# Optimization experiments

Hardware: AMD Instinct MI355X
Metric: run time of the kernel (lower is better)

Reference implementation:

```python
import jax, jax.numpy as jnp
import numpy as np
import math

B, L, I, H = 32, 2048, 64, 512
HALF = H // 2
DT = 0.05
RHO = 0.99
INPUT_SCALING = 1.0
STD = 1.0
GAMMA_MIN, GAMMA_MAX = 0.5, 1.0
EPS_MIN, EPS_MAX = 0.5, 1.0


def setup_inputs() -> dict:
    key = jax.random.key(0)
    ks = jax.random.split(key, 7)
    x = jax.random.normal(ks[0], (B, L, I), dtype=jnp.float32)
    x2h = jax.random.uniform(ks[1], (I, H), dtype=jnp.float32) * INPUT_SCALING
    h2h = 2.0 * (2.0 * jax.random.uniform(ks[2], (H, H), dtype=jnp.float32) - 1.0)
    # spectral_norm_scaling: rescale so largest singular value == rho
    h2h = h2h * (RHO / jnp.linalg.norm(h2h, ord=2))
    bias = (2.0 * jax.random.uniform(ks[3], (H,), dtype=jnp.float32) - 1.0) * INPUT_SCALING
    gamma = jax.random.uniform(ks[4], (H,), dtype=jnp.float32) * (GAMMA_MAX - GAMMA_MIN) + GAMMA_MIN
    epsilon = jax.random.uniform(ks[5], (H,), dtype=jnp.float32) * (EPS_MAX - EPS_MIN) + EPS_MIN
    # RandomFourierFeature: W_sin = W_cos, shape [half_dim, in_dim]
    W_rff = jax.random.normal(ks[6], (HALF, H), dtype=jnp.float32) * STD
    return {"x": x, "x2h": x2h, "h2h": h2h, "bias": bias,
            "gamma": gamma, "epsilon": epsilon, "W_rff": W_rff}


def _run(x, x2h, h2h, bias, gamma, epsilon, W_rff):
    b = x.shape[0]
    inv_sqrt_half = 1.0 / math.sqrt(HALF)

    def step(carry, xt):
        hy, hz, zsum = carry
        pre = jnp.tanh(xt @ x2h + hy @ h2h + bias)          # [B,H]
        hz = hz + DT * (pre - gamma * hy - epsilon * hz)
        hy = hy + DT * hz
        wx = hy @ W_rff.T                                   # [B,HALF]
        z = jnp.concatenate([jnp.cos(wx), jnp.sin(wx)], axis=-1) * inv_sqrt_half
        return (hy, hz, zsum + z), None

    hy0 = jnp.zeros((b, H), dtype=x.dtype)
    hz0 = jnp.zeros((b, H), dtype=x.dtype)
    zsum0 = jnp.zeros((b, H), dtype=x.dtype)
    (hy, hz, zsum), _ = jax.lax.scan(step, (hy0, hz0, zsum0), jnp.swapaxes(x, 0, 1))
    mu = zsum / x.shape[1]  # mean over time of per-step RFF states
    return mu, hy


def reference(x, x2h, h2h, bias, gamma, epsilon, W_rff):
    return _run(x, x2h, h2h, bias, gamma, epsilon, W_rff)
```

## Files before the change

### kernel.cpp

```cpp
#include <hip/hip_runtime.h>
#include <math.h>

#define Bz 32
#define Lz 2048
#define Iz 64
#define Hz 512
#define HALFz 256
#define DTz 0.05f
#define NMEM 8
#define TPB 512

typedef unsigned long long u64;

__device__ __forceinline__ bool tagok(u64 v, unsigned tag) {
  u64 want = (u64)tag | ((u64)tag << 48);
  return ((v ^ want) & 0xFFFF00000000FFFFull) == 0ull;
}
__device__ __forceinline__ u64 packv(float f, unsigned tag) {
  return (u64)tag | ((u64)__float_as_uint(f) << 16) | ((u64)tag << 48);
}
__device__ __forceinline__ float unpackv(u64 v) {
  return __uint_as_float((unsigned)(v >> 16));
}

__device__ __forceinline__ u64 load_sc0(const u64* p) {
  u64 r;
  asm volatile("global_load_dwordx2 %0, %1, off sc0\n\t"
               "s_waitcnt vmcnt(0)"
               : "=&v"(r) : "v"(p) : "memory");
  return r;
}
__device__ __forceinline__ void store_sc0(u64* p, u64 v) {
  asm volatile("global_store_dwordx2 %0, %1, off sc0"
               :: "v"(p), "v"(v) : "memory");
}

__global__ __launch_bounds__(TPB, 2) void coesn_sc0(
    const float* __restrict__ x, const float* __restrict__ x2h,
    const float* __restrict__ h2h, const float* __restrict__ bias,
    const float* __restrict__ gam, const float* __restrict__ eps,
    const float* __restrict__ W_rff, u64* __restrict__ Xb,
    u64* __restrict__ Yb, float* __restrict__ out) {
  __shared__ __align__(16) float hyf[2][Hz];
  __shared__ __align__(16) float xb[2][Iz];

  const int b  = blockIdx.x & 31;
  const int m  = blockIdx.x >> 5;
  const int u  = threadIdx.x;
  const int w  = u >> 6;
  const int l  = u & 63;
  const int c0 = m * 64;
  const int j  = ((l & 1) << 2) | (l & 2) | ((l >> 2) & 1);
  const int mycol = c0 + w * 8 + j;
  const int rloc = u >> 4, kseg = u & 15;

  float wreg[8][8];
  {
    const float* hrow = h2h + (size_t)(8 * l) * Hz + c0 + 8 * w;
    #pragma unroll
    for (int r = 0; r < 8; ++r) {
      float4 v0 = *(const float4*)(hrow + (size_t)r * Hz);
      float4 v1 = *(const float4*)(hrow + (size_t)r * Hz + 4);
      wreg[r][0] = v0.x; wreg[r][1] = v0.y; wreg[r][2] = v0.z; wreg[r][3] = v0.w;
      wreg[r][4] = v1.x; wreg[r][5] = v1.y; wreg[r][6] = v1.z; wreg[r][7] = v1.w;
    }
  }
  float xreg[8];
  {
    float4 v0 = *(const float4*)(x2h + (size_t)l * Hz + c0 + 8 * w);
    float4 v1 = *(const float4*)(x2h + (size_t)l * Hz + c0 + 8 * w + 4);
    xreg[0] = v0.x; xreg[1] = v0.y; xreg[2] = v0.z; xreg[3] = v0.w;
    xreg[4] = v1.x; xreg[5] = v1.y; xreg[6] = v1.z; xreg[7] = v1.w;
  }
  float wr[32];
  {
    const float* wp = W_rff + (size_t)(m * 32 + rloc) * Hz + kseg * 32;
    #pragma unroll
    for (int i = 0; i < 32; ++i) wr[i] = wp[i];
  }

  const float bu = bias[mycol];
  const float gu = gam[mycol];
  const float eu = eps[mycol];
  float hy = 0.f, hz = 0.f, zc = 0.f, zs = 0.f;
  hyf[0][u] = 0.f;
  if (u < 16) ((float4*)xb[0])[u] = ((const float4*)(x + (size_t)b * Lz * Iz))[u];
  __syncthreads();

  auto rff_acc = [&](const float* hsrc) {
    float acc = 0.f;
    const float4* hp = (const float4*)hsrc;
    #pragma unroll
    for (int i = 0; i < 8; ++i) {
      int q = kseg * 8 + i;
      float4 h4 = hp[q ^ ((q >> 3) & 7)];
      acc = fmaf(h4.x, wr[4 * i], acc);
      acc = fmaf(h4.y, wr[4 * i + 1], acc);
      acc = fmaf(h4.z, wr[4 * i + 2], acc);
      acc = fmaf(h4.w, wr[4 * i + 3], acc);
    }
    acc += __shfl_xor(acc, 1); acc += __shfl_xor(acc, 2);
    acc += __shfl_xor(acc, 4); acc += __shfl_xor(acc, 8);
    float sv, cv;
    __sincosf(acc, &sv, &cv);
    zc += cv; zs += sv;
  };

  for (int t = 0; t < Lz; ++t) {
    const int cur = t & 1, nxt = cur ^ 1;

    if (u < 16 && t + 1 < Lz)
      ((float4*)xb[nxt])[u] =
          ((const float4*)(x + ((size_t)b * Lz + (t + 1)) * Iz))[u];

    float hv[8];
    {
      const float4* hp = (const float4*)hyf[cur];
      int q0 = 2 * l, q1 = 2 * l + 1;
      float4 h0 = hp[q0 ^ ((q0 >> 3) & 7)];
      float4 h1 = hp[q1 ^ ((q1 >> 3) & 7)];
      hv[0] = h0.x; hv[1] = h0.y; hv[2] = h0.z; hv[3] = h0.w;
      hv[4] = h1.x; hv[5] = h1.y; hv[6] = h1.z; hv[7] = h1.w;
    }
    float a[8] = {0.f, 0.f, 0.f, 0.f, 0.f, 0.f, 0.f, 0.f};
    #pragma unroll
    for (int r = 0; r < 8; ++r) {
      float h = hv[r];
      #pragma unroll
      for (int c = 0; c < 8; ++c) a[c] = fmaf(h, wreg[r][c], a[c]);
    }
    {
      float xv = xb[cur][l];
      #pragma unroll
      for (int c = 0; c < 8; ++c) a[c] = fmaf(xv, xreg[c], a[c]);
    }
    #pragma unroll
    for (int i = 0; i < 4; ++i) {
      float snd = (l & 1) ? a[i] : a[i + 4];
      float rcv = __shfl_xor(snd, 1);
      a[i] = ((l & 1) ? a[i + 4] : a[i]) + rcv;
    }
    #pragma unroll
    for (int i = 0; i < 2; ++i) {
      float snd = (l & 2) ? a[i] : a[i + 2];
      float rcv = __shfl_xor(snd, 2);
      a[i] = ((l & 2) ? a[i + 2] : a[i]) + rcv;
    }
    float s;
    {
      float snd = (l & 4) ? a[0] : a[1];
      float rcv = __shfl_xor(snd, 4);
      s = ((l & 4) ? a[1] : a[0]) + rcv;
    }
    s += __shfl_xor(s, 8); s += __shfl_xor(s, 16); s += __shfl_xor(s, 32);

    s += bu;
    float e2 = __expf(s + s);
    float pre = 1.f - 2.f * __builtin_amdgcn_rcpf(e2 + 1.f);
    float hzn = fmaf(DTz, pre - gu * hy - eu * hz, hz);
    hy = fmaf(DTz, hzn, hy);
    hz = hzn;

    const unsigned tag = (unsigned)(t + 1);
    u64* XA = Xb + ((size_t)nxt * Bz + b) * Hz;
    u64* YA = Yb + ((size_t)nxt * Bz + b) * Hz;

    if (l < 8) {
      u64 pv = packv(hy, tag);
      store_sc0(XA + mycol, pv);
      __hip_atomic_store(YA + mycol, pv, __ATOMIC_RELAXED,
                         __HIP_MEMORY_SCOPE_AGENT);
      int q = mycol >> 2;
      hyf[nxt][((q ^ ((q >> 3) & 7)) << 2) | (mycol & 3)] = hy;
    }

    u64 spec = 0;
    if (w != m) {
      asm volatile("global_load_dwordx2 %0, %1, off sc0"
                   : "=&v"(spec) : "v"(XA + u) : "memory");
    }

    if (t > 0) rff_acc(hyf[cur]);

    if (w != m) {
      asm volatile("s_waitcnt vmcnt(0)" : "+v"(spec) :: "memory");
      u64 v = spec;
      if (!tagok(v, tag)) {
        int it = 0;
        for (;;) {
          v = load_sc0(XA + u);
          if (tagok(v, tag)) break;
          if (it >= 2) {
            v = __hip_atomic_load(YA + u, __ATOMIC_RELAXED,
                                  __HIP_MEMORY_SCOPE_AGENT);
            if (tagok(v, tag)) break;
          }
          if (++it > (1 << 20)) break;
        }
      }
      int q = u >> 2;
      hyf[nxt][((q ^ ((q >> 3) & 7)) << 2) | (u & 3)] = unpackv(v);
    }
    __syncthreads();
  }

  rff_acc(hyf[0]);

  if (l < 8) out[(size_t)Bz * Hz + (size_t)b * Hz + mycol] = hy;
  if (kseg == 0) {
    const float sc = 0.0625f / 2048.f;
    out[(size_t)b * Hz + m * 32 + rloc] = zc * sc;
    out[(size_t)b * Hz + HALFz + m * 32 + rloc] = zs * sc;
  }
}

#define FMA4(P, S, W) do { (P).x = fmaf((S), (W).x, (P).x); (P).y = fmaf((S), (W).y, (P).y); \
                           (P).z = fmaf((S), (W).z, (P).z); (P).w = fmaf((S), (W).w, (P).w); } while(0)

__global__ __launch_bounds__(512) void coesn_scan_fb(
    const float* __restrict__ x, const float* __restrict__ x2h,
    const float* __restrict__ h2h, const float* __restrict__ bias,
    const float* __restrict__ gam, const float* __restrict__ eps,
    const float* __restrict__ W_rff, float* __restrict__ out) {
  const int b = blockIdx.x;
  const int u = threadIdx.x;
  __shared__ __align__(16) float hy_lds[Hz];
  __shared__ __align__(16) float x_lds[Iz];
  __shared__ float4 part[4][128];
  __shared__ float wx_lds[HALFz];

  float hy = 0.f, hz = 0.f, zsum = 0.f;
  const float bu = bias[u];
  const float gu = gam[u];
  const float eu = eps[u];

  const int kq = u >> 7;
  const int g  = u & 127;
  const int jj = u >> 2;
  const int ks = u & 3;

  const float4* __restrict__ H4 = (const float4*)h2h;
  const float4* __restrict__ X2 = (const float4*)x2h;
  const float4* __restrict__ W4 = (const float4*)W_rff;
  const float4* __restrict__ XG = (const float4*)x;
  const float4* hy4 = (const float4*)hy_lds;

  hy_lds[u] = 0.f;
  if (u < 16) ((float4*)x_lds)[u] = XG[(long)b * Lz * 16 + u];
  __syncthreads();

  for (int t = 0; t < Lz; ++t) {
    float4 p = make_float4(0.f, 0.f, 0.f, 0.f);
    {
      const float4* hp = (const float4*)&hy_lds[kq << 7];
      #pragma unroll 8
      for (int k4 = 0; k4 < 32; ++k4) {
        float4 hv = hp[k4];
        const float4* wr2 = &H4[(size_t)((kq << 7) + (k4 << 2)) * 128 + g];
        float4 w0 = wr2[0]; float4 w1 = wr2[128]; float4 w2 = wr2[256]; float4 w3 = wr2[384];
        FMA4(p, hv.x, w0); FMA4(p, hv.y, w1); FMA4(p, hv.z, w2); FMA4(p, hv.w, w3);
      }
      const float4* xp = (const float4*)&x_lds[kq << 4];
      #pragma unroll
      for (int k4 = 0; k4 < 4; ++k4) {
        float4 xv = xp[k4];
        const float4* wr2 = &X2[(size_t)((kq << 4) + (k4 << 2)) * 128 + g];
        float4 w0 = wr2[0]; float4 w1 = wr2[128]; float4 w2 = wr2[256]; float4 w3 = wr2[384];
        FMA4(p, xv.x, w0); FMA4(p, xv.y, w1); FMA4(p, xv.z, w2); FMA4(p, xv.w, w3);
      }
    }
    part[kq][g] = p;
    __syncthreads();
    {
      const float* pp = (const float*)part;
      float s = (pp[u] + pp[512 + u]) + (pp[1024 + u] + pp[1536 + u]);
      float pre = tanhf(s + bu);
      float hzn = fmaf(DTz, pre - gu * hy - eu * hz, hz);
      hy = fmaf(DTz, hzn, hy);
      hz = hzn;
      hy_lds[u] = hy;
      if (u < 16 && t + 1 < Lz)
        ((float4*)x_lds)[u] = XG[((long)b * Lz + (t + 1)) * 16 + u];
    }
    __syncthreads();
    {
      float4 acc0 = make_float4(0.f,0.f,0.f,0.f), acc1 = make_float4(0.f,0.f,0.f,0.f);
      #pragma unroll 4
      for (int it = 0; it < 32; ++it) {
        int k4 = (it << 2) + ks;
        float4 hv = hy4[k4];
        float4 w0 = W4[(size_t)jj * 128 + k4];
        float4 w1 = W4[(size_t)(jj + 128) * 128 + k4];
        acc0.x = fmaf(hv.x, w0.x, acc0.x); acc0.y = fmaf(hv.y, w0.y, acc0.y);
        acc0.z = fmaf(hv.z, w0.z, acc0.z); acc0.w = fmaf(hv.w, w0.w, acc0.w);
        acc1.x = fmaf(hv.x, w1.x, acc1.x); acc1.y = fmaf(hv.y, w1.y, acc1.y);
        acc1.z = fmaf(hv.z, w1.z, acc1.z); acc1.w = fmaf(hv.w, w1.w, acc1.w);
      }
      float a0 = (acc0.x + acc0.y) + (acc0.z + acc0.w);
      float a1 = (acc1.x + acc1.y) + (acc1.z + acc1.w);
      a0 += __shfl_xor(a0, 1); a0 += __shfl_xor(a0, 2);
      a1 += __shfl_xor(a1, 1); a1 += __shfl_xor(a1, 2);
      if (ks == 0) { wx_lds[jj] = a0; wx_lds[jj + 128] = a1; }
    }
    __syncthreads();
    {
      float v = wx_lds[u & 255];
      zsum += (u < HALFz) ? cosf(v) : sinf(v);
    }
  }
  out[(long)b * Hz + u] = zsum * (0.0625f / 2048.f);
  out[(long)Bz * Hz + (long)b * Hz + u] = hy;
}

extern "C" void kernel_launch(void* const* d_in, const int* in_sizes, int n_in,
                              void* d_out, int out_size, void* d_ws, size_t ws_size,
                              hipStream_t stream) {
  const float* x    = (const float*)d_in[0];
  const float* x2h  = (const float*)d_in[1];
  const float* h2h  = (const float*)d_in[2];
  const float* bias = (const float*)d_in[3];
  const float* gam  = (const float*)d_in[4];
  const float* eps  = (const float*)d_in[5];
  const float* wrff = (const float*)d_in[6];
  float* out = (float*)d_out;

  const size_t NEX = (size_t)2 * Bz * Hz;
  const size_t WS_NEED = 2 * NEX * sizeof(u64);
  if (ws_size >= WS_NEED) {
    u64* Xb = (u64*)d_ws;
    u64* Yb = Xb + NEX;
    hipMemsetAsync(d_ws, 0, WS_NEED, stream);
    void* args[] = { (void*)&x, (void*)&x2h, (void*)&h2h, (void*)&bias,
                     (void*)&gam, (void*)&eps, (void*)&wrff,
                     (void*)&Xb, (void*)&Yb, (void*)&out };
    hipError_t e = hipLaunchCooperativeKernel((const void*)coesn_sc0,
                                              dim3(Bz * NMEM), dim3(TPB),
                                              args, 0, stream);
    if (e == hipSuccess) return;
  }
  coesn_scan_fb<<<Bz, 512, 0, stream>>>(x, x2h, h2h, bias, gam, eps, wrff, out);
}
```

Before: 3.510 ms.

## Process two batch rows per block to halve grid and overlap chains

Each block now handles a pair of batch elements, so the grid shrinks from 256 to 128 blocks. The h2h weight registers are reused for both recurrences, and one batch's global exchange latency can overlap the other batch's compute. The cost is roughly twice the per-step serial work per block. Launch bounds drop to one block per CU, which may hurt latency hiding.

```diff
diff --git a/kernel.cpp b/kernel.cpp
--- a/kernel.cpp
+++ b/kernel.cpp
@@ -8,6 +8,7 @@
 #define HALFz 256
 #define DTz 0.05f
 #define NMEM 8
+#define NPAIR 16
 #define TPB 512
 
 typedef unsigned long long u64;
@@ -35,17 +36,20 @@
                :: "v"(p), "v"(v) : "memory");
 }
 
-__global__ __launch_bounds__(TPB, 2) void coesn_sc0(
+__global__ __launch_bounds__(TPB, 1) void coesn_2c(
     const float* __restrict__ x, const float* __restrict__ x2h,
     const float* __restrict__ h2h, const float* __restrict__ bias,
     const float* __restrict__ gam, const float* __restrict__ eps,
     const float* __restrict__ W_rff, u64* __restrict__ Xb,
     u64* __restrict__ Yb, float* __restrict__ out) {
-  __shared__ __align__(16) float hyf[2][Hz];
-  __shared__ __align__(16) float xb[2][Iz];
-
-  const int b  = blockIdx.x & 31;
-  const int m  = blockIdx.x >> 5;
+  __shared__ __align__(16) float hyfA[2][Hz];
+  __shared__ __align__(16) float hyfB[2][Hz];
+  __shared__ __align__(16) float xbA[2][Iz];
+  __shared__ __align__(16) float xbB[2][Iz];
+
+  const int p  = blockIdx.x & 15;
+  const int m  = blockIdx.x >> 4;
+  const int bA = 2 * p, bB = 2 * p + 1;
   const int u  = threadIdx.x;
   const int w  = u >> 6;
   const int l  = u & 63;
@@ -82,12 +86,68 @@
   const float bu = bias[mycol];
   const float gu = gam[mycol];
   const float eu = eps[mycol];
-  float hy = 0.f, hz = 0.f, zc = 0.f, zs = 0.f;
-  hyf[0][u] = 0.f;
-  if (u < 16) ((float4*)xb[0])[u] = ((const float4*)(x + (size_t)b * Lz * Iz))[u];
+  float hyA = 0.f, hzA = 0.f, zcA = 0.f, zsA = 0.f;
+  float hyB = 0.f, hzB = 0.f, zcB = 0.f, zsB = 0.f;
+  hyfA[0][u] = 0.f; hyfB[0][u] = 0.f;
+  if (u < 16) ((float4*)xbA[0])[u] = ((const float4*)(x + (size_t)bA * Lz * Iz))[u];
+  else if (u >= 64 && u < 80)
+    ((float4*)xbB[0])[u - 64] = ((const float4*)(x + (size_t)bB * Lz * Iz))[u - 64];
   __syncthreads();
 
-  auto rff_acc = [&](const float* hsrc) {
+  auto matvec = [&](const float* hcur, const float* xcur) -> float {
+    float hv[8];
+    {
+      const float4* hp = (const float4*)hcur;
+      int q0 = 2 * l, q1 = 2 * l + 1;
+      float4 h0 = hp[q0 ^ ((q0 >> 3) & 7)];
+      float4 h1 = hp[q1 ^ ((q1 >> 3) & 7)];
+      hv[0] = h0.x; hv[1] = h0.y; hv[2] = h0.z; hv[3] = h0.w;
+      hv[4] = h1.x; hv[5] = h1.y; hv[6] = h1.z; hv[7] = h1.w;
+    }
+    float a[8] = {0.f,0.f,0.f,0.f,0.f,0.f,0.f,0.f};
+    #pragma unroll
+    for (int r = 0; r < 8; ++r) {
+      float h = hv[r];
+      #pragma unroll
+      for (int c = 0; c < 8; ++c) a[c] = fmaf(h, wreg[r][c], a[c]);
+    }
+    {
+      float xv = xcur[l];
+      #pragma unroll
+      for (int c = 0; c < 8; ++c) a[c] = fmaf(xv, xreg[c], a[c]);
+    }
+    #pragma unroll
+    for (int i = 0; i < 4; ++i) {
+      float snd = (l & 1) ? a[i] : a[i + 4];
+      float rcv = __shfl_xor(snd, 1);
+      a[i] = ((l & 1) ? a[i + 4] : a[i]) + rcv;
+    }
+    #pragma unroll
+    for (int i = 0; i < 2; ++i) {
+      float snd = (l & 2) ? a[i] : a[i + 2];
+      float rcv = __shfl_xor(snd, 2);
+      a[i] = ((l & 2) ? a[i + 2] : a[i]) + rcv;
+    }
+    float s;
+    {
+      float snd = (l & 4) ? a[0] : a[1];
+      float rcv = __shfl_xor(snd, 4);
+      s = ((l & 4) ? a[1] : a[0]) + rcv;
+    }
+    s += __shfl_xor(s, 8); s += __shfl_xor(s, 16); s += __shfl_xor(s, 32);
+    return s;
+  };
+
+  auto update = [&](float s, float& hy, float& hz) {
+    s += bu;
+    float e2 = __expf(s + s);
+    float pre = 1.f - 2.f * __builtin_amdgcn_rcpf(e2 + 1.f);
+    float hzn = fmaf(DTz, pre - gu * hy - eu * hz, hz);
+    hy = fmaf(DTz, hzn, hy);
+    hz = hzn;
+  };
+
+  auto rff_acc = [&](const float* hsrc, float& zc, float& zs) {
     float acc = 0.f;
     const float4* hp = (const float4*)hsrc;
     #pragma unroll
@@ -106,111 +166,106 @@
     zc += cv; zs += sv;
   };
 
+  auto validate = [&](u64 spec, u64* XA, u64* YA, unsigned tag,
+                      float (*hyf)[Hz], int nxt) {
+    u64 v = spec;
+    if (!tagok(v, tag)) {
+      int it = 0;
+      for (;;) {
+        v = load_sc0(XA + u);
+        if (tagok(v, tag)) break;
+        if (it >= 2) {
+          v = __hip_atomic_load(YA + u, __ATOMIC_RELAXED,
+                                __HIP_MEMORY_SCOPE_AGENT);
+          if (tagok(v, tag)) break;
+        }
+        if (++it > (1 << 20)) break;
+      }
+    }
+    int q = u >> 2;
+    hyf[nxt][((q ^ ((q >> 3) & 7)) << 2) | (u & 3)] = unpackv(v);
+  };
+
   for (int t = 0; t < Lz; ++t) {
     const int cur = t & 1, nxt = cur ^ 1;
-
-    if (u < 16 && t + 1 < Lz)
-      ((float4*)xb[nxt])[u] =
-          ((const float4*)(x + ((size_t)b * Lz + (t + 1)) * Iz))[u];
-
-    float hv[8];
-    {
-      const float4* hp = (const float4*)hyf[cur];
-      int q0 = 2 * l, q1 = 2 * l + 1;
-      float4 h0 = hp[q0 ^ ((q0 >> 3) & 7)];
-      float4 h1 = hp[q1 ^ ((q1 >> 3) & 7)];
-      hv[0] = h0.x; hv[1] = h0.y; hv[2] = h0.z; hv[3] = h0.w;
-      hv[4] = h1.x; hv[5] = h1.y; hv[6] = h1.z; hv[7] = h1.w;
-    }
-    float a[8] = {0.f, 0.f, 0.f, 0.f, 0.f, 0.f, 0.f, 0.f};
-    #pragma unroll
-    for (int r = 0; r < 8; ++r) {
-      float h = hv[r];
-      #pragma unroll
-      for (int c = 0; c < 8; ++c) a[c] = fmaf(h, wreg[r][c], a[c]);
-    }
-    {
-      float xv = xb[cur][l];
-      #pragma unroll
-      for (int c = 0; c < 8; ++c) a[c] = fmaf(xv, xreg[c], a[c]);
-    }
-    #pragma unroll
-    for (int i = 0; i < 4; ++i) {
-      float snd = (l & 1) ? a[i] : a[i + 4];
-      float rcv = __shfl_xor(snd, 1);
-      a[i] = ((l & 1) ? a[i + 4] : a[i]) + rcv;
-    }
-    #pragma unroll
-    for (int i = 0; i < 2; ++i) {
-      float snd = (l & 2) ? a[i] : a[i + 2];
-      float rcv = __shfl_xor(snd, 2);
-      a[i] = ((l & 2) ? a[i + 2] : a[i]) + rcv;
-    }
-    float s;
-    {
-      float snd = (l & 4) ? a[0] : a[1];
-      float rcv = __shfl_xor(snd, 4);
-      s = ((l & 4) ? a[1] : a[0]) + rcv;
-    }
-    s += __shfl_xor(s, 8); s += __shfl_xor(s, 16); s += __shfl_xor(s, 32);
-
-    s += bu;
-    float e2 = __expf(s + s);
-    float pre = 1.f - 2.f * __builtin_amdgcn_rcpf(e2 + 1.f);
-    float hzn = fmaf(DTz, pre - gu * hy - eu * hz, hz);
-    hy = fmaf(DTz, hzn, hy);
-    hz = hzn;
-
     const unsigned tag = (unsigned)(t + 1);
-    u64* XA = Xb + ((size_t)nxt * Bz + b) * Hz;
-    u64* YA = Yb + ((size_t)nxt * Bz + b) * Hz;
-
-    if (l < 8) {
-      u64 pv = packv(hy, tag);
-      store_sc0(XA + mycol, pv);
-      __hip_atomic_store(YA + mycol, pv, __ATOMIC_RELAXED,
-                         __HIP_MEMORY_SCOPE_AGENT);
-      int q = mycol >> 2;
-      hyf[nxt][((q ^ ((q >> 3) & 7)) << 2) | (mycol & 3)] = hy;
-    }
-
-    u64 spec = 0;
+    u64* XAa = Xb + ((size_t)nxt * Bz + bA) * Hz;
+    u64* YAa = Yb + ((size_t)nxt * Bz + bA) * Hz;
+    u64* XAb = Xb + ((size_t)nxt * Bz + bB) * Hz;
+    u64* YAb = Yb + ((size_t)nxt * Bz + bB) * Hz;
+
+    if (t + 1 < Lz) {
+      if (u < 16)
+        ((float4*)xbA[nxt])[u] = ((const float4*)(x + ((size_t)bA * Lz + t + 1) * Iz))[u];
+      else if (u >= 64 && u < 80)
+        ((float4*)xbB[nxt])[u - 64] = ((const float4*)(x + ((size_t)bB * Lz + t + 1) * Iz))[u - 64];
+    }
+
+    {
+      float s = matvec(hyfA[cur], xbA[cur]);
+      update(s, hyA, hzA);
+      if (l < 8) {
+        u64 pv = packv(hyA, tag);
+        store_sc0(XAa + mycol, pv);
+        __hip_atomic_store(YAa + mycol, pv, __ATOMIC_RELAXED,
+                           __HIP_MEMORY_SCOPE_AGENT);
+        int q = mycol >> 2;
+        hyfA[nxt][((q ^ ((q >> 3) & 7)) << 2) | (mycol & 3)] = hyA;
+      }
+    }
+
+    {
+      float s = matvec(hyfB[cur], xbB[cur]);
+      update(s, hyB, hzB);
+      if (l < 8) {
+        u64 pv = packv(hyB, tag);
+        store_sc0(XAb + mycol, pv);
+        __hip_atomic_store(YAb + mycol, pv, __ATOMIC_RELAXED,
+                           __HIP_MEMORY_SCOPE_AGENT);
+        int q = mycol >> 2;
+        hyfB[nxt][((q ^ ((q >> 3) & 7)) << 2) | (mycol & 3)] = hyB;
+      }
+    }
+
+    u64 specA = 0;
+    if (w != m)
+      asm volatile("global_load_dwordx2 %0, %1, off sc0"
+                   : "=&v"(specA) : "v"(XAa + u) : "memory");
+
+    if (t > 0) rff_acc(hyfA[cur], zcA, zsA);
+
     if (w != m) {
+      asm volatile("s_waitcnt vmcnt(0)" : "+v"(specA) :: "memory");
+      validate(specA, XAa, YAa, tag, hyfA, nxt);
+    }
+
+    u64 specB = 0;
+    if (w != m)
       asm volatile("global_load_dwordx2 %0, %1, off sc0"
-                   : "=&v"(spec) : "v"(XA + u) : "memory");
-    }
-
-    if (t > 0) rff_acc(hyf[cur]);
+                   : "=&v"(specB) : "v"(XAb + u) : "memory");
+
+    if (t > 0) rff_acc(hyfB[cur], zcB, zsB);
 
     if (w != m) {
-      asm volatile("s_waitcnt vmcnt(0)" : "+v"(spec) :: "memory");
-      u64 v = spec;
-      if (!tagok(v, tag)) {
-        int it = 0;
-        for (;;) {
-          v = load_sc0(XA + u);
-          if (tagok(v, tag)) break;
-          if (it >= 2) {
-            v = __hip_atomic_load(YA + u, __ATOMIC_RELAXED,
-                                  __HIP_MEMORY_SCOPE_AGENT);
-            if (tagok(v, tag)) break;
-          }
-          if (++it > (1 << 20)) break;
-        }
-      }
-      int q = u >> 2;
-      hyf[nxt][((q ^ ((q >> 3) & 7)) << 2) | (u & 3)] = unpackv(v);
+      asm volatile("s_waitcnt vmcnt(0)" : "+v"(specB) :: "memory");
+      validate(specB, XAb, YAb, tag, hyfB, nxt);
     }
     __syncthreads();
   }
 
-  rff_acc(hyf[0]);
-
-  if (l < 8) out[(size_t)Bz * Hz + (size_t)b * Hz + mycol] = hy;
+  rff_acc(hyfA[0], zcA, zsA);
+  rff_acc(hyfB[0], zcB, zsB);
+
+  if (l < 8) {
+    out[(size_t)Bz * Hz + (size_t)bA * Hz + mycol] = hyA;
+    out[(size_t)Bz * Hz + (size_t)bB * Hz + mycol] = hyB;
+  }
   if (kseg == 0) {
     const float sc = 0.0625f / 2048.f;
-    out[(size_t)b * Hz + m * 32 + rloc] = zc * sc;
-    out[(size_t)b * Hz + HALFz + m * 32 + rloc] = zs * sc;
+    out[(size_t)bA * Hz + m * 32 + rloc] = zcA * sc;
+    out[(size_t)bA * Hz + HALFz + m * 32 + rloc] = zsA * sc;
+    out[(size_t)bB * Hz + m * 32 + rloc] = zcB * sc;
+    out[(size_t)bB * Hz + HALFz + m * 32 + rloc] = zsB * sc;
   }
 }
 
@@ -333,8 +388,8 @@
     void* args[] = { (void*)&x, (void*)&x2h, (void*)&h2h, (void*)&bias,
                      (void*)&gam, (void*)&eps, (void*)&wrff,
                      (void*)&Xb, (void*)&Yb, (void*)&out };
-    hipError_t e = hipLaunchCooperativeKernel((const void*)coesn_sc0,
-                                              dim3(Bz * NMEM), dim3(TPB),
+    hipError_t e = hipLaunchCooperativeKernel((const void*)coesn_2c,
+                                              dim3(NMEM * NPAIR), dim3(TPB),
                                               args, 0, stream);
     if (e == hipSuccess) return;
   }
```

Result: slower. 6.940 ms (+97.7%).

## Place each batch's block group on one XCD via runtime XCC-id assignment

Applied to the files above, without the earlier changes.

Adds a new cooperative kernel in which each block reads its XCC id from a hardware register and takes a global ticket. It then remaps itself to a (batch, member) pair so the 8 blocks exchanging hidden state for one batch sit on the same XCD where possible. It also requests 96KB of dynamic LDS to force one block per CU and reorders the speculative exchange load before the atomic store, waiting with vmcnt(1). This is meant to cut cross-XCD coherence latency in the per-timestep inter-block exchange, at the cost of a startup barrier and dependence on a spin-based grid rendezvous.

```diff
diff --git a/kernel.cpp b/kernel.cpp
--- a/kernel.cpp
+++ b/kernel.cpp
@@ -8,6 +8,7 @@
 #define HALFz 256
 #define DTz 0.05f
 #define NMEM 8
+#define NBLK 256
 #define TPB 512
 
 typedef unsigned long long u64;
@@ -35,7 +36,219 @@
                :: "v"(p), "v"(v) : "memory");
 }
 
-__global__ __launch_bounds__(TPB, 2) void coesn_sc0(
+__global__ __launch_bounds__(TPB, 1) void coesn_xg(
+    const float* __restrict__ x, const float* __restrict__ x2h,
+    const float* __restrict__ h2h, const float* __restrict__ bias,
+    const float* __restrict__ gam, const float* __restrict__ eps,
+    const float* __restrict__ W_rff, unsigned* __restrict__ regs,
+    u64* __restrict__ Xb, u64* __restrict__ Yb, float* __restrict__ out) {
+  extern __shared__ float lds_force[];
+  __shared__ __align__(16) float hyf[2][Hz];
+  __shared__ __align__(16) float xbuf[2][Iz];
+  __shared__ int sbm[2];
+
+  const int u = threadIdx.x;
+
+  if (u == 0) {
+    unsigned xcc = __builtin_amdgcn_s_getreg((31 << 11) | 20) & 7u;
+    unsigned idx = __hip_atomic_fetch_add(regs + xcc, 1u, __ATOMIC_RELAXED,
+                                          __HIP_MEMORY_SCOPE_AGENT);
+    __hip_atomic_fetch_add(regs + 32, 1u, __ATOMIC_RELEASE,
+                           __HIP_MEMORY_SCOPE_AGENT);
+    unsigned v;
+    do { v = __hip_atomic_load(regs + 32, __ATOMIC_ACQUIRE,
+                               __HIP_MEMORY_SCOPE_AGENT); } while (v < NBLK);
+    unsigned n[8], full[8], rem[8], totf = 0;
+    for (int i = 0; i < 8; ++i) {
+      n[i] = __hip_atomic_load(regs + i, __ATOMIC_RELAXED,
+                               __HIP_MEMORY_SCOPE_AGENT);
+      full[i] = n[i] >> 3; rem[i] = n[i] & 7; totf += full[i];
+    }
+    int gid, mem;
+    if (idx < 8u * full[xcc]) {
+      unsigned pf = 0;
+      for (unsigned i = 0; i < xcc; ++i) pf += full[i];
+      gid = (int)(pf + (idx >> 3)); mem = (int)(idx & 7u);
+    } else {
+      unsigned pr = 0;
+      for (unsigned i = 0; i < xcc; ++i) pr += rem[i];
+      unsigned rank = pr + (idx - 8u * full[xcc]);
+      gid = (int)(totf + (rank >> 3)); mem = (int)(rank & 7u);
+    }
+    sbm[0] = gid; sbm[1] = mem;
+  }
+  __syncthreads();
+  const int b = sbm[0];
+  const int m = sbm[1];
+
+  const int w  = u >> 6;
+  const int l  = u & 63;
+  const int c0 = m * 64;
+  const int j  = ((l & 1) << 2) | (l & 2) | ((l >> 2) & 1);
+  const int mycol = c0 + w * 8 + j;
+  const int rloc = u >> 4, kseg = u & 15;
+
+  float wreg[8][8];
+  {
+    const float* hrow = h2h + (size_t)(8 * l) * Hz + c0 + 8 * w;
+    #pragma unroll
+    for (int r = 0; r < 8; ++r) {
+      float4 v0 = *(const float4*)(hrow + (size_t)r * Hz);
+      float4 v1 = *(const float4*)(hrow + (size_t)r * Hz + 4);
+      wreg[r][0] = v0.x; wreg[r][1] = v0.y; wreg[r][2] = v0.z; wreg[r][3] = v0.w;
+      wreg[r][4] = v1.x; wreg[r][5] = v1.y; wreg[r][6] = v1.z; wreg[r][7] = v1.w;
+    }
+  }
+  float xreg[8];
+  {
+    float4 v0 = *(const float4*)(x2h + (size_t)l * Hz + c0 + 8 * w);
+    float4 v1 = *(const float4*)(x2h + (size_t)l * Hz + c0 + 8 * w + 4);
+    xreg[0] = v0.x; xreg[1] = v0.y; xreg[2] = v0.z; xreg[3] = v0.w;
+    xreg[4] = v1.x; xreg[5] = v1.y; xreg[6] = v1.z; xreg[7] = v1.w;
+  }
+  float wr[32];
+  {
+    const float* wp = W_rff + (size_t)(m * 32 + rloc) * Hz + kseg * 32;
+    #pragma unroll
+    for (int i = 0; i < 32; ++i) wr[i] = wp[i];
+  }
+
+  const float bu = bias[mycol];
+  const float gu = gam[mycol];
+  const float eu = eps[mycol];
+  float hy = 0.f, hz = 0.f, zc = 0.f, zs = 0.f;
+  hyf[0][u] = 0.f;
+  if (u < 16) ((float4*)xbuf[0])[u] = ((const float4*)(x + (size_t)b * Lz * Iz))[u];
+  __syncthreads();
+
+  auto rff_acc = [&](const float* hsrc) {
+    float acc = 0.f;
+    const float4* hp = (const float4*)hsrc;
+    #pragma unroll
+    for (int i = 0; i < 8; ++i) {
+      int q = kseg * 8 + i;
+      float4 h4 = hp[q ^ ((q >> 3) & 7)];
+      acc = fmaf(h4.x, wr[4 * i], acc);
+      acc = fmaf(h4.y, wr[4 * i + 1], acc);
+      acc = fmaf(h4.z, wr[4 * i + 2], acc);
+      acc = fmaf(h4.w, wr[4 * i + 3], acc);
+    }
+    acc += __shfl_xor(acc, 1); acc += __shfl_xor(acc, 2);
+    acc += __shfl_xor(acc, 4); acc += __shfl_xor(acc, 8);
+    float sv, cv;
+    __sincosf(acc, &sv, &cv);
+    zc += cv; zs += sv;
+  };
+
+  for (int t = 0; t < Lz; ++t) {
+    const int cur = t & 1, nxt = cur ^ 1;
+
+    if (u < 16 && t + 1 < Lz)
+      ((float4*)xbuf[nxt])[u] =
+          ((const float4*)(x + ((size_t)b * Lz + (t + 1)) * Iz))[u];
+
+    float hv[8];
+    {
+      const float4* hp = (const float4*)hyf[cur];
+      int q0 = 2 * l, q1 = 2 * l + 1;
+      float4 h0 = hp[q0 ^ ((q0 >> 3) & 7)];
+      float4 h1 = hp[q1 ^ ((q1 >> 3) & 7)];
+      hv[0] = h0.x; hv[1] = h0.y; hv[2] = h0.z; hv[3] = h0.w;
+      hv[4] = h1.x; hv[5] = h1.y; hv[6] = h1.z; hv[7] = h1.w;
+    }
+    float a[8] = {0.f,0.f,0.f,0.f,0.f,0.f,0.f,0.f};
+    #pragma unroll
+    for (int r = 0; r < 8; ++r) {
+      float h = hv[r];
+      #pragma unroll
+      for (int c = 0; c < 8; ++c) a[c] = fmaf(h, wreg[r][c], a[c]);
+    }
+    {
+      float xv = xbuf[cur][l];
+      #pragma unroll
+      for (int c = 0; c < 8; ++c) a[c] = fmaf(xv, xreg[c], a[c]);
+    }
+    #pragma unroll
+    for (int i = 0; i < 4; ++i) {
+      float snd = (l & 1) ? a[i] : a[i + 4];
+      float rcv = __shfl_xor(snd, 1);
+      a[i] = ((l & 1) ? a[i + 4] : a[i]) + rcv;
+    }
+    #pragma unroll
+    for (int i = 0; i < 2; ++i) {
+      float snd = (l & 2) ? a[i] : a[i + 2];
+      float rcv = __shfl_xor(snd, 2);
+      a[i] = ((l & 2) ? a[i + 2] : a[i]) + rcv;
+    }
+    float s;
+    {
+      float snd = (l & 4) ? a[0] : a[1];
+      float rcv = __shfl_xor(snd, 4);
+      s = ((l & 4) ? a[1] : a[0]) + rcv;
+    }
+    s += __shfl_xor(s, 8); s += __shfl_xor(s, 16); s += __shfl_xor(s, 32);
+
+    s += bu;
+    float e2 = __expf(s + s);
+    float pre = 1.f - 2.f * __builtin_amdgcn_rcpf(e2 + 1.f);
+    float hzn = fmaf(DTz, pre - gu * hy - eu * hz, hz);
+    hy = fmaf(DTz, hzn, hy);
+    hz = hzn;
+
+    const unsigned tag = (unsigned)(t + 1);
+    u64* XA = Xb + ((size_t)nxt * Bz + b) * Hz;
+    u64* YA = Yb + ((size_t)nxt * Bz + b) * Hz;
+
+    u64 pv = packv(hy, tag);
+    if (l < 8) store_sc0(XA + mycol, pv);
+
+    u64 spec = 0;
+    if (w != m)
+      asm volatile("global_load_dwordx2 %0, %1, off sc0"
+                   : "=&v"(spec) : "v"(XA + u) : "memory");
+
+    if (l < 8) {
+      __hip_atomic_store(YA + mycol, pv, __ATOMIC_RELAXED,
+                         __HIP_MEMORY_SCOPE_AGENT);
+      int q = mycol >> 2;
+      hyf[nxt][((q ^ ((q >> 3) & 7)) << 2) | (mycol & 3)] = hy;
+    }
+
+    if (t > 0) rff_acc(hyf[cur]);
+
+    if (w != m) {
+      asm volatile("s_waitcnt vmcnt(1)" : "+v"(spec) :: "memory");
+      u64 v = spec;
+      if (!tagok(v, tag)) {
+        long it = 0;
+        for (;;) {
+          v = load_sc0(XA + u);
+          if (tagok(v, tag)) break;
+          if (it & 1) {
+            v = __hip_atomic_load(YA + u, __ATOMIC_RELAXED,
+                                  __HIP_MEMORY_SCOPE_AGENT);
+            if (tagok(v, tag)) break;
+          }
+          if (++it > (1 << 20)) break;
+        }
+      }
+      int q = u >> 2;
+      hyf[nxt][((q ^ ((q >> 3) & 7)) << 2) | (u & 3)] = unpackv(v);
+    }
+    __syncthreads();
+  }
+
+  rff_acc(hyf[0]);
+
+  if (l < 8) out[(size_t)Bz * Hz + (size_t)b * Hz + mycol] = hy;
+  if (kseg == 0) {
+    const float sc = 0.0625f / 2048.f;
+    out[(size_t)b * Hz + m * 32 + rloc] = zc * sc;
+    out[(size_t)b * Hz + HALFz + m * 32 + rloc] = zs * sc;
+  }
+}
+
+__global__ __launch_bounds__(TPB, 2) void coesn_x2(
     const float* __restrict__ x, const float* __restrict__ x2h,
     const float* __restrict__ h2h, const float* __restrict__ bias,
     const float* __restrict__ gam, const float* __restrict__ eps,
@@ -108,11 +321,9 @@
 
   for (int t = 0; t < Lz; ++t) {
     const int cur = t & 1, nxt = cur ^ 1;
-
     if (u < 16 && t + 1 < Lz)
       ((float4*)xb[nxt])[u] =
           ((const float4*)(x + ((size_t)b * Lz + (t + 1)) * Iz))[u];
-
     float hv[8];
     {
       const float4* hp = (const float4*)hyf[cur];
@@ -122,7 +333,7 @@
       hv[0] = h0.x; hv[1] = h0.y; hv[2] = h0.z; hv[3] = h0.w;
       hv[4] = h1.x; hv[5] = h1.y; hv[6] = h1.z; hv[7] = h1.w;
     }
-    float a[8] = {0.f, 0.f, 0.f, 0.f, 0.f, 0.f, 0.f, 0.f};
+    float a[8] = {0.f,0.f,0.f,0.f,0.f,0.f,0.f,0.f};
     #pragma unroll
     for (int r = 0; r < 8; ++r) {
       float h = hv[r];
@@ -167,36 +378,24 @@
 
     if (l < 8) {
       u64 pv = packv(hy, tag);
-      store_sc0(XA + mycol, pv);
+      *(volatile u64*)(XA + mycol) = pv;
       __hip_atomic_store(YA + mycol, pv, __ATOMIC_RELAXED,
                          __HIP_MEMORY_SCOPE_AGENT);
       int q = mycol >> 2;
       hyf[nxt][((q ^ ((q >> 3) & 7)) << 2) | (mycol & 3)] = hy;
     }
-
-    u64 spec = 0;
+    if (t > 0) rff_acc(hyf[cur]);
     if (w != m) {
-      asm volatile("global_load_dwordx2 %0, %1, off sc0"
-                   : "=&v"(spec) : "v"(XA + u) : "memory");
-    }
-
-    if (t > 0) rff_acc(hyf[cur]);
-
-    if (w != m) {
-      asm volatile("s_waitcnt vmcnt(0)" : "+v"(spec) :: "memory");
-      u64 v = spec;
-      if (!tagok(v, tag)) {
-        int it = 0;
-        for (;;) {
-          v = load_sc0(XA + u);
+      u64 v; int it = 0;
+      for (;;) {
+        v = *(volatile const u64*)(XA + u);
+        if (tagok(v, tag)) break;
+        if (it >= 2) {
+          v = __hip_atomic_load(YA + u, __ATOMIC_RELAXED,
+                                __HIP_MEMORY_SCOPE_AGENT);
           if (tagok(v, tag)) break;
-          if (it >= 2) {
-            v = __hip_atomic_load(YA + u, __ATOMIC_RELAXED,
-                                  __HIP_MEMORY_SCOPE_AGENT);
-            if (tagok(v, tag)) break;
-          }
-          if (++it > (1 << 20)) break;
         }
+        if (++it > (1 << 20)) break;
       }
       int q = u >> 2;
       hyf[nxt][((q ^ ((q >> 3) & 7)) << 2) | (u & 3)] = unpackv(v);
@@ -205,7 +404,6 @@
   }
 
   rff_acc(hyf[0]);
-
   if (l < 8) out[(size_t)Bz * Hz + (size_t)b * Hz + mycol] = hy;
   if (kseg == 0) {
     const float sc = 0.0625f / 2048.f;
@@ -325,18 +523,35 @@
   float* out = (float*)d_out;
 
   const size_t NEX = (size_t)2 * Bz * Hz;
-  const size_t WS_NEED = 2 * NEX * sizeof(u64);
+  const size_t WS_NEED = 4096 + 2 * NEX * sizeof(u64);
+  const unsigned DYN_LDS = 96 * 1024;
+
   if (ws_size >= WS_NEED) {
-    u64* Xb = (u64*)d_ws;
+    unsigned* regs = (unsigned*)d_ws;
+    u64* Xb = (u64*)((char*)d_ws + 4096);
     u64* Yb = Xb + NEX;
     hipMemsetAsync(d_ws, 0, WS_NEED, stream);
-    void* args[] = { (void*)&x, (void*)&x2h, (void*)&h2h, (void*)&bias,
-                     (void*)&gam, (void*)&eps, (void*)&wrff,
-                     (void*)&Xb, (void*)&Yb, (void*)&out };
-    hipError_t e = hipLaunchCooperativeKernel((const void*)coesn_sc0,
-                                              dim3(Bz * NMEM), dim3(TPB),
-                                              args, 0, stream);
-    if (e == hipSuccess) return;
+
+    hipError_t ea = hipFuncSetAttribute((const void*)coesn_xg,
+                                        hipFuncAttributeMaxDynamicSharedMemorySize,
+                                        (int)DYN_LDS);
+    if (ea == hipSuccess) {
+      void* args[] = { (void*)&x, (void*)&x2h, (void*)&h2h, (void*)&bias,
+                       (void*)&gam, (void*)&eps, (void*)&wrff,
+                       (void*)&regs, (void*)&Xb, (void*)&Yb, (void*)&out };
+      hipError_t e = hipLaunchCooperativeKernel((const void*)coesn_xg,
+                                                dim3(NBLK), dim3(TPB),
+                                                args, DYN_LDS, stream);
+      if (e == hipSuccess) return;
+    }
+
+    void* args2[] = { (void*)&x, (void*)&x2h, (void*)&h2h, (void*)&bias,
+                      (void*)&gam, (void*)&eps, (void*)&wrff,
+                      (void*)&Xb, (void*)&Yb, (void*)&out };
+    hipError_t e2 = hipLaunchCooperativeKernel((const void*)coesn_x2,
+                                               dim3(Bz * NMEM), dim3(TPB),
+                                               args2, 0, stream);
+    if (e2 == hipSuccess) return;
   }
   coesn_scan_fb<<<Bz, 512, 0, stream>>>(x, x2h, h2h, bias, gam, eps, wrff, out);
 }
```

After: 3.621 ms. +3.2%, slower.
